# Performance work log

Hardware: AMD Instinct MI355X
Metric: run time of the kernel (lower is better)

## Reference

```python
import jax, jax.numpy as jnp
import numpy as np

K = 20
EPS = 1e-5
NEG_SLOPE = 0.2


def knn_idx(pts, k):
    # pts: [B, N, C] -> indices of k nearest neighbors [B, N, k]
    sq = jnp.sum(pts * pts, axis=-1)                     # [B, N]
    inner = jnp.einsum('bnc,bmc->bnm', pts, pts)         # [B, N, N]
    dist = sq[:, :, None] - 2.0 * inner + sq[:, None, :] # [B, N, N]
    _, idx = jax.lax.top_k(-dist, k)                     # nearest = smallest dist
    return idx


def batchnorm(h, gamma, beta):
    # h: [B, N, k, C]; normalize over (B, N, k) per channel (training-mode stats)
    mean = jnp.mean(h, axis=(0, 1, 2), keepdims=True)
    var = jnp.var(h, axis=(0, 1, 2), keepdims=True)
    return gamma * (h - mean) * jax.lax.rsqrt(var + EPS) + beta


def setup_inputs() -> dict:
    key = jax.random.key(0)
    ks = jax.random.split(key, 7)
    B, C, N = 8, 3, 4096
    x = jax.random.normal(ks[0], (B, C, N), dtype=jnp.float32)
    W1 = jax.random.normal(ks[1], (64, 6), dtype=jnp.float32) * (1.0 / np.sqrt(6.0))
    gamma1 = jnp.ones((64,), dtype=jnp.float32)
    beta1 = jnp.zeros((64,), dtype=jnp.float32)
    W2 = jax.random.normal(ks[2], (64, 64), dtype=jnp.float32) * (1.0 / 8.0)
    gamma2 = jnp.ones((64,), dtype=jnp.float32)
    beta2 = jnp.zeros((64,), dtype=jnp.float32)
    return {"x": x, "W1": W1, "gamma1": gamma1, "beta1": beta1,
            "W2": W2, "gamma2": gamma2, "beta2": beta2}


def reference(x, W1, gamma1, beta1, W2, gamma2, beta2):
    # x: [B, 3, N] point cloud
    pts = jnp.transpose(x, (0, 2, 1))                    # [B, N, 3]
    idx = knn_idx(pts, K)                                # [B, N, k]
    nbr = jax.vmap(lambda p, i: p[i])(pts, idx)          # [B, N, k, 3]
    center = pts[:, :, None, :]                          # [B, N, 1, 3]
    edge = jnp.concatenate(
        [nbr - center, jnp.broadcast_to(center, nbr.shape)], axis=-1)  # [B, N, k, 6]

    h = jnp.einsum('bnkc,oc->bnko', edge, W1)            # [B, N, k, 64]
    h = jax.nn.leaky_relu(batchnorm(h, gamma1, beta1), NEG_SLOPE)
    h = jnp.einsum('bnkc,oc->bnko', h, W2)               # [B, N, k, 64]
    h = jax.nn.leaky_relu(batchnorm(h, gamma2, beta2), NEG_SLOPE)

    out = jnp.max(h, axis=2)                             # max-pool over k neighbors
    return jnp.transpose(out, (0, 2, 1))                 # [B, 64, N]
```

## Files before the change

kernel.cpp:

```cpp
#include <hip/hip_runtime.h>
#include <hip/hip_bf16.h>
#include <math.h>

#define BB 8
#define NN 4096
#define KNN 20
#define CH 64
#define SAMPLES (BB*NN*KNN)
#define EPSF 1e-5f
#define SLOPE 0.2f
#define MCOPY 32

typedef float f32x4 __attribute__((ext_vector_type(4)));
typedef short bf16x8 __attribute__((ext_vector_type(8)));

__device__ __forceinline__ float key_decode(unsigned e) {
    return __uint_as_float((e & 0x80000000u) ? (e ^ 0x80000000u) : ~e);
}

__device__ __forceinline__ void rank_flush(unsigned long long* ovf,
                                           unsigned long long* inc,
                                           unsigned long long* scr,
                                           int& cnt, float& kthd, int lane) {
    while (cnt > 0) {
        int take = cnt < 44 ? cnt : 44;
        unsigned long long key;
        if (lane < take)      key = ovf[cnt - take + lane];
        else if (lane >= 44)  key = inc[lane - 44];
        else                  key = ~0ull;
        scr[lane] = key;
        __builtin_amdgcn_wave_barrier();
        int r = 0;
#pragma unroll
        for (int t = 0; t < 64; ++t) {
            unsigned long long kt = scr[t];
            r += (kt < key) ? 1 : 0;
        }
        __builtin_amdgcn_wave_barrier();
        if (r < KNN) inc[r] = key;
        __builtin_amdgcn_wave_barrier();
        kthd = key_decode((unsigned)(inc[KNN-1] >> 32));
        cnt -= take;
    }
}

__global__ __launch_bounds__(1024) void sort_kernel(const float* __restrict__ x,
        float4* __restrict__ pts4, float4* __restrict__ sp4, int* __restrict__ sidx,
        int* __restrict__ rankArr, double* __restrict__ zreg) {
#pragma clang fp contract(off)
    __shared__ unsigned long long S[NN];
    const int tid = threadIdx.x;
    const int b = blockIdx.x;
    if (b == 0 && tid < 992) zreg[tid] = 0.0;
    const float* xb = x + (size_t)b * 3 * NN;
    for (int i = tid; i < NN; i += 1024) {
        float mx = xb[i], my = xb[NN + i], mz = xb[2*NN + i];
        float sq = mx*mx; sq += my*my; sq += mz*mz;
        pts4[(b << 12) + i] = make_float4(-2.0f*mx, -2.0f*my, -2.0f*mz, sq);
        unsigned uu = __float_as_uint(mx);
        unsigned e = uu ^ (((unsigned)((int)uu >> 31)) | 0x80000000u);
        S[i] = ((unsigned long long)e << 32) | (unsigned)i;
    }
    __syncthreads();
    for (int k = 2; k <= NN; k <<= 1) {
        for (int j = k >> 1; j > 0; j >>= 1) {
#pragma unroll
            for (int tt = 0; tt < 2; ++tt) {
                int t = tid + tt*1024;
                int i = ((t & ~(j - 1)) << 1) | (t & (j - 1));
                int h = i | j;
                unsigned long long a = S[i], c = S[h];
                bool up = ((i & k) == 0);
                if ((a > c) == up) { S[i] = c; S[h] = a; }
            }
            __syncthreads();
        }
    }
    for (int s = tid; s < NN; s += 1024) {
        int oi = (int)(unsigned)(S[s] & 0xFFFFFFFFu);
        float mx = xb[oi], my = xb[NN + oi], mz = xb[2*NN + oi];
        float sq = mx*mx; sq += my*my; sq += mz*mz;
        sp4[(b << 12) + s] = make_float4(-2.0f*mx, -2.0f*my, -2.0f*mz, sq);
        sidx[(b << 12) + s] = oi;
        rankArr[(b << 12) + oi] = s;
    }
}

__global__ __launch_bounds__(256) void knn_kernel(const float4* __restrict__ pts4,
        const float4* __restrict__ sp4, const int* __restrict__ sidx,
        int* __restrict__ idx_out, double* __restrict__ mstats) {
#pragma clang fp contract(off)
    __shared__ unsigned long long OVF[4][160];
    __shared__ unsigned long long INC[4][24];
    __shared__ unsigned long long SCR[4][64];
    __shared__ float MOM[4][27];
    const int tid = threadIdx.x;
    const int lane = tid & 63;
    const int wv = __builtin_amdgcn_readfirstlane(tid >> 6);
    const int s = blockIdx.x * 4 + wv;
    const int b = s >> 12;
    const int ss = s & (NN - 1);
    const float4* sb = sp4 + ((size_t)b << 12);
    const int* si = sidx + ((size_t)b << 12);
    unsigned long long* ovf = &OVF[wv][0];
    unsigned long long* inc = &INC[wv][0];
    unsigned long long* scr = &SCR[wv][0];

    const float4 Qc = sb[ss];
    const float qx = -0.5f*Qc.x, qy = -0.5f*Qc.y, qz = -0.5f*Qc.z;
    const float sqn = Qc.w;
    int c0 = ss - 32; c0 = c0 < 0 ? 0 : (c0 > NN-64 ? NN-64 : c0);
    float kthd, thr, M;
    int cnt = 0;

    {
        const float4 P = sb[c0 + lane];
        const float mx = -0.5f*P.x, my = -0.5f*P.y, mz = -0.5f*P.z;
        float inner = qx*mx; inner += qy*my; inner += qz*mz;
        const float d = (sqn - 2.0f*inner) + P.w;
        unsigned uu = __float_as_uint(d);
        unsigned e = uu ^ (((unsigned)((int)uu >> 31)) | 0x80000000u);
        unsigned long long key = ((unsigned long long)e << 32) | (unsigned)si[c0 + lane];
        scr[lane] = key;
        __builtin_amdgcn_wave_barrier();
        int r = 0;
#pragma unroll
        for (int t = 0; t < 64; ++t) {
            unsigned long long kt = scr[t];
            r += (kt < key) ? 1 : 0;
        }
        __builtin_amdgcn_wave_barrier();
        if (r < KNN) inc[r] = key;
        __builtin_amdgcn_wave_barrier();
        kthd = key_decode((unsigned)(inc[KNN-1] >> 32));
        M = 1e-3f*(fabsf(kthd) + fabsf(sqn) + 1.0f);
        thr = (kthd - sqn) + M;
    }

    int lo = c0, hi = c0 + 64;
    bool dl = (lo == 0), dr = (hi == NN);

    float4 PL, PR;
    float xL = 0.f, xR = 0.f;
    if (!dl) {
        int st = lo - 64; st = st < 0 ? 0 : st;
        PL = sb[st + lane];
        xL = sb[lo - 1].x;
    }
    if (!dr) {
        int sI = hi + lane;
        PR = sb[sI < NN-1 ? sI : NN-1];
        xR = sb[hi].x;
    }

    while (!dl || !dr) {
        bool goL = false, goR = false;
        if (!dl) {
            const float dx = qx - (-0.5f*xL);
            goL = (dx*dx <= kthd + M);
            if (!goL) dl = true;
        }
        if (!dr) {
            const float dx = (-0.5f*xR) - qx;
            goR = (dx*dx <= kthd + M);
            if (!goR) dr = true;
        }
        const int stL = (lo - 64) < 0 ? 0 : (lo - 64);
        const int enR = (hi + 64) > NN ? NN : (hi + 64);

        float4 PLn = PL, PRn = PR;
        float xLn = 0.f, xRn = 0.f;
        if (goL && stL > 0) {
            int st2 = stL - 64; st2 = st2 < 0 ? 0 : st2;
            PLn = sb[st2 + lane];
            xLn = sb[stL - 1].x;
        }
        if (goR && enR < NN) {
            int sI = enR + lane;
            PRn = sb[sI < NN-1 ? sI : NN-1];
            xRn = sb[enR].x;
        }

        if (cnt > 32) {
            rank_flush(ovf, inc, scr, cnt, kthd, lane);
            M = 1e-3f*(fabsf(kthd) + fabsf(sqn) + 1.0f);
            thr = (kthd - sqn) + M;
        }

        if (goL) {
            const int sI = stL + lane;
            const bool valid = sI < lo;
            const float sc = fmaf(PL.x, qx, fmaf(PL.y, qy, fmaf(PL.z, qz, PL.w)));
            bool push = valid && (sc <= thr);
            unsigned long long mask = __ballot(push);
            if (mask) {
                if (push) {
                    const float mx = -0.5f*PL.x, my = -0.5f*PL.y, mz = -0.5f*PL.z;
                    float inner = qx*mx; inner += qy*my; inner += qz*mz;
                    const float d = (sqn - 2.0f*inner) + PL.w;
                    unsigned uu = __float_as_uint(d);
                    unsigned e = uu ^ (((unsigned)((int)uu >> 31)) | 0x80000000u);
                    unsigned long long key = ((unsigned long long)e << 32) | (unsigned)si[sI];
                    int ofs = (int)__popcll(mask & ((1ull << lane) - 1ull));
                    ovf[cnt + ofs] = key;
                }
                cnt += (int)__popcll(mask);
            }
            lo = stL;
            dl = (lo == 0);
            PL = PLn; xL = xLn;
        }
        if (goR) {
            const int sI = hi + lane;
            const int sa = sI < NN-1 ? sI : NN-1;
            const bool valid = sI < enR;
            const float sc = fmaf(PR.x, qx, fmaf(PR.y, qy, fmaf(PR.z, qz, PR.w)));
            bool push = valid && (sc <= thr);
            unsigned long long mask = __ballot(push);
            if (mask) {
                if (push) {
                    const float mx = -0.5f*PR.x, my = -0.5f*PR.y, mz = -0.5f*PR.z;
                    float inner = qx*mx; inner += qy*my; inner += qz*mz;
                    const float d = (sqn - 2.0f*inner) + PR.w;
                    unsigned uu = __float_as_uint(d);
                    unsigned e = uu ^ (((unsigned)((int)uu >> 31)) | 0x80000000u);
                    unsigned long long key = ((unsigned long long)e << 32) | (unsigned)si[sa];
                    int ofs = (int)__popcll(mask & ((1ull << lane) - 1ull));
                    ovf[cnt + ofs] = key;
                }
                cnt += (int)__popcll(mask);
            }
            hi = enR;
            dr = (hi == NN);
            PR = PRn; xR = xRn;
        }
    }
    rank_flush(ovf, inc, scr, cnt, kthd, lane);

    if (lane < KNN)
        idx_out[(size_t)s * KNN + lane] = (int)(unsigned)(inc[lane] & 0xFFFFFFFFull);

    float nx = 0.f, ny = 0.f, nz = 0.f, xx = 0.f, xy = 0.f, xz = 0.f,
          yy = 0.f, yz = 0.f, zz = 0.f;
    if (lane < KNN) {
        int nbr = (int)(unsigned)(inc[lane] & 0xFFFFFFFFull);
        float4 pn = pts4[(b << 12) + nbr];
        nx = -0.5f*pn.x; ny = -0.5f*pn.y; nz = -0.5f*pn.z;
        xx = nx*nx; xy = nx*ny; xz = nx*nz; yy = ny*ny; yz = ny*nz; zz = nz*nz;
    }
#pragma unroll
    for (int off = 32; off > 0; off >>= 1) {
        nx += __shfl_xor(nx, off); ny += __shfl_xor(ny, off); nz += __shfl_xor(nz, off);
        xx += __shfl_xor(xx, off); xy += __shfl_xor(xy, off); xz += __shfl_xor(xz, off);
        yy += __shfl_xor(yy, off); yz += __shfl_xor(yz, off); zz += __shfl_xor(zz, off);
    }
    if (lane == 0) {
        MOM[wv][0] = nx;  MOM[wv][1] = ny;  MOM[wv][2] = nz;
        MOM[wv][3] = qx;  MOM[wv][4] = qy;  MOM[wv][5] = qz;
        MOM[wv][6] = xx;  MOM[wv][7] = xy;  MOM[wv][8] = xz;
        MOM[wv][9] = yy;  MOM[wv][10] = yz; MOM[wv][11] = zz;
        MOM[wv][12] = nx*qx; MOM[wv][13] = nx*qy; MOM[wv][14] = nx*qz;
        MOM[wv][15] = ny*qx; MOM[wv][16] = ny*qy; MOM[wv][17] = ny*qz;
        MOM[wv][18] = nz*qx; MOM[wv][19] = nz*qy; MOM[wv][20] = nz*qz;
        MOM[wv][21] = qx*qx; MOM[wv][22] = qx*qy; MOM[wv][23] = qx*qz;
        MOM[wv][24] = qy*qy; MOM[wv][25] = qy*qz; MOM[wv][26] = qz*qz;
    }
    __syncthreads();
    if (tid < 27)
        atomicAdd(&mstats[(blockIdx.x & (MCOPY-1))*27 + tid],
                  (double)(MOM[0][tid] + MOM[1][tid] + MOM[2][tid] + MOM[3][tid]));
}

__device__ __forceinline__ void bsplit(float g, short& hi, short& lo) {
    unsigned bits = __float_as_uint(g);
    unsigned hbits = bits & 0xFFFF0000u;
    float rem = g - __uint_as_float(hbits);
    hi = (short)(bits >> 16);
    lo = (short)(__float_as_uint(rem) >> 16);
}

__global__ __launch_bounds__(256) void main_kernel(const int* __restrict__ idxb,
        const int* __restrict__ rankArr, const float4* __restrict__ pts4,
        const double* __restrict__ ms, const float* __restrict__ W1,
        const float* __restrict__ gamma1, const float* __restrict__ beta1,
        const float* __restrict__ W2,
        float* __restrict__ maxbuf, float* __restrict__ stats2f) {
    __shared__ __align__(16) short Thi[4][32*72];
    __shared__ __align__(16) short Tlo[4][32*72];
    __shared__ float chs[128];
    __shared__ float ab1s[128];
    __shared__ double msd[27];
    const int tid = threadIdx.x;
    const int lane = tid & 63;
    const int wv = __builtin_amdgcn_readfirstlane(tid >> 6);
    const int l15 = lane & 15;
    const int quad = lane >> 4;
    if (tid < 128) chs[tid] = 0.f;
    if (tid < 27) {
        double t = 0.0;
        for (int c = 0; c < MCOPY; ++c) t += ms[c*27 + tid];
        msd[tid] = t;
    }
    __syncthreads();
    if (tid < 64) {
        int c = tid;
        double wu[3], wvv[3];
#pragma unroll
        for (int i = 0; i < 3; ++i) {
            wu[i] = (double)W1[c*6 + i];
            wvv[i] = (double)W1[c*6 + 3 + i] - wu[i];
        }
        const double S = (double)SAMPLES;
        double mean = (wu[0]*msd[0] + wu[1]*msd[1] + wu[2]*msd[2]
                     + 20.0*(wvv[0]*msd[3] + wvv[1]*msd[4] + wvv[2]*msd[5])) / S;
        double qM1 = wu[0]*wu[0]*msd[6] + wu[1]*wu[1]*msd[9] + wu[2]*wu[2]*msd[11]
                   + 2.0*(wu[0]*wu[1]*msd[7] + wu[0]*wu[2]*msd[8] + wu[1]*wu[2]*msd[10]);
        double cross = 0.0;
#pragma unroll
        for (int i = 0; i < 3; ++i)
#pragma unroll
            for (int j = 0; j < 3; ++j)
                cross += wu[i] * msd[12 + i*3 + j] * wvv[j];
        double qpp = wvv[0]*wvv[0]*msd[21] + wvv[1]*wvv[1]*msd[24] + wvv[2]*wvv[2]*msd[26]
                   + 2.0*(wvv[0]*wvv[1]*msd[22] + wvv[0]*wvv[2]*msd[23] + wvv[1]*wvv[2]*msd[25]);
        double e2 = (qM1 + 2.0*cross + 20.0*qpp) / S;
        double var = e2 - mean*mean;
        float a = (float)((double)gamma1[c] / sqrt(var + (double)EPSF));
        ab1s[c] = a;
        ab1s[64 + c] = beta1[c] - a * (float)mean;
    }
    __syncthreads();

    bf16x8 whi[8], wlo[8];
#pragma unroll
    for (int t = 0; t < 4; ++t)
#pragma unroll
    for (int f = 0; f < 2; ++f) {
        const int o = 16*t + l15;
        const int c0 = 32*f + quad*8;
        const float4* wr = (const float4*)(W2 + o*64 + c0);
        float4 w0 = wr[0], w1 = wr[1];
        float vals[8] = {w0.x,w0.y,w0.z,w0.w,w1.x,w1.y,w1.z,w1.w};
        bf16x8 h, l;
#pragma unroll
        for (int j = 0; j < 8; ++j) { short hj, lj; bsplit(vals[j], hj, lj); h[j]=hj; l[j]=lj; }
        whi[t*2+f] = h; wlo[t*2+f] = l;
    }

    const float w10 = W1[lane*6+0], w11 = W1[lane*6+1], w12 = W1[lane*6+2];
    const float w13 = W1[lane*6+3], w14 = W1[lane*6+4], w15 = W1[lane*6+5];
    const float a1 = ab1s[lane], b1 = ab1s[64 + lane];
    float ssum[4] = {0.f,0.f,0.f,0.f}, ssq[4] = {0.f,0.f,0.f,0.f};
    float lm[4][4];
    short* thi = &Thi[wv][0];
    short* tlo = &Tlo[wv][0];

    const int pt0 = (blockIdx.x * 4 + wv) * 4;
    const int b = pt0 >> 12;
    const float4* pb = pts4 + ((size_t)b << 12);
    const int* rnk = rankArr + ((size_t)b << 12);

    for (int p = 0; p < 4; ++p) {
        const int pt = pt0 + p;
        const float4 pc = pb[pt & (NN - 1)];
        const float X = -0.5f*pc.x, Y = -0.5f*pc.y, Z = -0.5f*pc.z;
        const float vc = (w13 - w10)*X + (w14 - w11)*Y + (w15 - w12)*Z;
        const int srow = rnk[pt & (NN - 1)];
        const int* irow = idxb + ((size_t)((b << 12) + srow)) * KNN;
#pragma unroll
        for (int k = 0; k < KNN; ++k) {
            float4 pn = pb[irow[k]];
            float nx = -0.5f*pn.x, ny = -0.5f*pn.y, nz = -0.5f*pn.z;
            float uc = w10*nx + w11*ny + w12*nz;
            float g = a1 * (uc + vc) + b1;
            g = fmaxf(g, SLOPE * g);
            short hj, lj; bsplit(g, hj, lj);
            const int row = (k < 16) ? k : (16 + p*4 + (k - 16));
            thi[row*72 + lane] = hj;
            tlo[row*72 + lane] = lj;
        }
        __builtin_amdgcn_wave_barrier();

        bf16x8 ah1[2], al1[2];
#pragma unroll
        for (int f = 0; f < 2; ++f) {
            const int co = 32*f + quad*8;
            ah1[f] = *(const bf16x8*)&thi[l15*72 + co];
            al1[f] = *(const bf16x8*)&tlo[l15*72 + co];
        }

        f32x4 acc1[4];
#pragma unroll
        for (int t = 0; t < 4; ++t) acc1[t] = (f32x4)0.f;
#pragma unroll
        for (int t = 0; t < 4; ++t) {
#pragma unroll
            for (int f = 0; f < 2; ++f) {
                acc1[t] = __builtin_amdgcn_mfma_f32_16x16x32_bf16(ah1[f], whi[t*2+f], acc1[t], 0,0,0);
                acc1[t] = __builtin_amdgcn_mfma_f32_16x16x32_bf16(al1[f], whi[t*2+f], acc1[t], 0,0,0);
                acc1[t] = __builtin_amdgcn_mfma_f32_16x16x32_bf16(ah1[f], wlo[t*2+f], acc1[t], 0,0,0);
            }
        }
        __builtin_amdgcn_wave_barrier();

#pragma unroll
        for (int t = 0; t < 4; ++t) {
            float m1 = fmaxf(fmaxf(acc1[t][0], acc1[t][1]), fmaxf(acc1[t][2], acc1[t][3]));
            float s1 = acc1[t][0] + acc1[t][1] + acc1[t][2] + acc1[t][3];
            float q1 = acc1[t][0]*acc1[t][0] + acc1[t][1]*acc1[t][1]
                     + acc1[t][2]*acc1[t][2] + acc1[t][3]*acc1[t][3];
            m1 = fmaxf(m1, __shfl_xor(m1, 16)); m1 = fmaxf(m1, __shfl_xor(m1, 32));
            s1 += __shfl_xor(s1, 16); s1 += __shfl_xor(s1, 32);
            q1 += __shfl_xor(q1, 16); q1 += __shfl_xor(q1, 32);
            lm[p][t] = m1;
            ssum[t] += s1; ssq[t] += q1;
        }
    }

    {
        bf16x8 ah2[2], al2[2];
#pragma unroll
        for (int f = 0; f < 2; ++f) {
            const int co = 32*f + quad*8;
            ah2[f] = *(const bf16x8*)&thi[(16 + l15)*72 + co];
            al2[f] = *(const bf16x8*)&tlo[(16 + l15)*72 + co];
        }
        f32x4 accC[4];
#pragma unroll
        for (int t = 0; t < 4; ++t) accC[t] = (f32x4)0.f;
#pragma unroll
        for (int t = 0; t < 4; ++t) {
#pragma unroll
            for (int f = 0; f < 2; ++f) {
                accC[t] = __builtin_amdgcn_mfma_f32_16x16x32_bf16(ah2[f], whi[t*2+f], accC[t], 0,0,0);
                accC[t] = __builtin_amdgcn_mfma_f32_16x16x32_bf16(al2[f], whi[t*2+f], accC[t], 0,0,0);
                accC[t] = __builtin_amdgcn_mfma_f32_16x16x32_bf16(ah2[f], wlo[t*2+f], accC[t], 0,0,0);
            }
        }
#pragma unroll
        for (int t = 0; t < 4; ++t) {
            float cm = fmaxf(fmaxf(accC[t][0], accC[t][1]), fmaxf(accC[t][2], accC[t][3]));
            float cs = accC[t][0] + accC[t][1] + accC[t][2] + accC[t][3];
            float cq = accC[t][0]*accC[t][0] + accC[t][1]*accC[t][1]
                     + accC[t][2]*accC[t][2] + accC[t][3]*accC[t][3];
            float lmq = (quad == 0) ? lm[0][t] : (quad == 1) ? lm[1][t]
                      : (quad == 2) ? lm[2][t] : lm[3][t];
            maxbuf[((size_t)(pt0 + quad) << 6) + 16*t + l15] = fmaxf(lmq, cm);
            cs += __shfl_xor(cs, 16); cs += __shfl_xor(cs, 32);
            cq += __shfl_xor(cq, 16); cq += __shfl_xor(cq, 32);
            ssum[t] += cs; ssq[t] += cq;
        }
    }

    if (quad == 0) {
#pragma unroll
        for (int t = 0; t < 4; ++t) {
            atomicAdd(&chs[16*t + l15], ssum[t]);
            atomicAdd(&chs[64 + 16*t + l15], ssq[t]);
        }
    }
    __syncthreads();
    if (tid < 128)
        atomicAdd(&stats2f[(blockIdx.x & 1)*128 + tid], chs[tid]);
}

__global__ __launch_bounds__(256) void out_kernel(const float* __restrict__ maxbuf,
        const float* __restrict__ s2f, const float* __restrict__ gamma2,
        const float* __restrict__ beta2, float* __restrict__ out) {
    __shared__ float t[64][65];
    __shared__ float ab2s[128];
    const int tid = threadIdx.x;
    if (tid < 64) {
        int o = tid;
        double sum = (double)s2f[o] + (double)s2f[128 + o];
        double sq  = (double)s2f[64 + o] + (double)s2f[192 + o];
        double cnt = (double)SAMPLES;
        double mean = sum / cnt;
        double var  = sq / cnt - mean*mean;
        float a = (float)((double)gamma2[o] / sqrt(var + (double)EPSF));
        ab2s[o] = a;
        ab2s[64 + o] = beta2[o] - a * (float)mean;
    }
    const int b = blockIdx.x >> 6;
    const int n0 = (blockIdx.x & 63) << 6;
#pragma unroll
    for (int i = 0; i < 16; ++i) {
        int r = (tid >> 6) + i*4;
        int c = tid & 63;
        t[r][c] = maxbuf[(((size_t)((b << 12) + n0 + r)) << 6) + c];
    }
    __syncthreads();
#pragma unroll
    for (int i = 0; i < 16; ++i) {
        int o = (tid >> 6) + i*4;
        int nn = tid & 63;
        float a = ab2s[o], bb = ab2s[64 + o];
        float h = a * t[nn][o] + bb;
        out[(((size_t)(b*64 + o)) << 12) + n0 + nn] = h >= 0.f ? h : SLOPE*h;
    }
}

extern "C" void kernel_launch(void* const* d_in, const int* in_sizes, int n_in,
                              void* d_out, int out_size, void* d_ws, size_t ws_size,
                              hipStream_t stream) {
    const float* x      = (const float*)d_in[0];
    const float* W1     = (const float*)d_in[1];
    const float* gamma1 = (const float*)d_in[2];
    const float* beta1  = (const float*)d_in[3];
    const float* W2     = (const float*)d_in[4];
    const float* gamma2 = (const float*)d_in[5];
    const float* beta2  = (const float*)d_in[6];
    float* out = (float*)d_out;

    char* ws = (char*)d_ws;
    int*    idxb    = (int*)   (ws + 0);
    float4* pts4    = (float4*)(ws + 2621440);
    float4* sp4     = (float4*)(ws + 3145728);
    int*    sidx    = (int*)   (ws + 3670016);
    int*    rankArr = (int*)   (ws + 3801088);
    float*  maxbuf  = (float*) (ws + 19398656);
    double* mstats  = (double*)(ws + 27787264);
    float*  stats2f = (float*) (ws + 27794176);
    double* zreg    = (double*)(ws + 27787264);

    sort_kernel <<<8, 1024, 0, stream>>>(x, pts4, sp4, sidx, rankArr, zreg);
    knn_kernel  <<<8192, 256, 0, stream>>>(pts4, sp4, sidx, idxb, mstats);
    main_kernel <<<2048, 256, 0, stream>>>(idxb, rankArr, pts4, mstats, W1, gamma1,
                                           beta1, W2, maxbuf, stats2f);
    out_kernel  <<<512, 256, 0, stream>>>(maxbuf, stats2f, gamma2, beta2, out);
}
```

Baseline: 256.8 us.

## Map one kNN query per lane with shared candidate chunks and per-lane insertion sort

The kNN kernel changes from one wave per query, with lanes as candidates and a 64-way rank sort for merging, to one wave handling 64 consecutive sorted queries, one per lane. Candidate chunks of 64 points are staged in LDS and scanned by every lane. Survivors go into a per-lane buffer that is merged into a per-lane top-20 list by insertion sort. The aim is to drop the cross-lane rank passes and the per-query scheduling overhead. The cost is wider union windows across queries, divergent insertion sorts, a large LDS footprint and only 512 single-wave blocks, which leaves the GPU lightly occupied.

Result: slower. 665.3 us (+159.0%).

```diff
diff --git a/kernel.cpp b/kernel.cpp
--- a/kernel.cpp
+++ b/kernel.cpp
@@ -16,32 +16,6 @@
 
 __device__ __forceinline__ float key_decode(unsigned e) {
     return __uint_as_float((e & 0x80000000u) ? (e ^ 0x80000000u) : ~e);
-}
-
-__device__ __forceinline__ void rank_flush(unsigned long long* ovf,
-                                           unsigned long long* inc,
-                                           unsigned long long* scr,
-                                           int& cnt, float& kthd, int lane) {
-    while (cnt > 0) {
-        int take = cnt < 44 ? cnt : 44;
-        unsigned long long key;
-        if (lane < take)      key = ovf[cnt - take + lane];
-        else if (lane >= 44)  key = inc[lane - 44];
-        else                  key = ~0ull;
-        scr[lane] = key;
-        __builtin_amdgcn_wave_barrier();
-        int r = 0;
-#pragma unroll
-        for (int t = 0; t < 64; ++t) {
-            unsigned long long kt = scr[t];
-            r += (kt < key) ? 1 : 0;
-        }
-        __builtin_amdgcn_wave_barrier();
-        if (r < KNN) inc[r] = key;
-        __builtin_amdgcn_wave_barrier();
-        kthd = key_decode((unsigned)(inc[KNN-1] >> 32));
-        cnt -= take;
-    }
 }
 
 __global__ __launch_bounds__(1024) void sort_kernel(const float* __restrict__ x,
@@ -86,189 +60,190 @@
     }
 }
 
-__global__ __launch_bounds__(256) void knn_kernel(const float4* __restrict__ pts4,
+
+#define BCAP 80
+
+__device__ __forceinline__ void lane_flush(unsigned long long* BUF,
+        unsigned long long* INC, const int lane, int& cnt, int& m,
+        float& kthd, const float sqn, float& M, float& thr) {
+    for (int j = 0; j < cnt; ++j) {
+        unsigned long long key = BUF[(j << 6) + lane];
+        if (m < KNN) {
+            int i = m - 1;
+            while (i >= 0 && INC[(i << 6) + lane] > key) {
+                INC[((i + 1) << 6) + lane] = INC[(i << 6) + lane]; --i;
+            }
+            INC[((i + 1) << 6) + lane] = key; ++m;
+        } else if (key < INC[((KNN - 1) << 6) + lane]) {
+            int i = KNN - 2;
+            while (i >= 0 && INC[(i << 6) + lane] > key) {
+                INC[((i + 1) << 6) + lane] = INC[(i << 6) + lane]; --i;
+            }
+            INC[((i + 1) << 6) + lane] = key;
+        }
+    }
+    cnt = 0;
+    if (m == KNN) {
+        kthd = key_decode((unsigned)(INC[((KNN - 1) << 6) + lane] >> 32));
+        M = 1e-3f*(fabsf(kthd) + fabsf(sqn) + 1.0f);
+        thr = (kthd - sqn) + M;
+    }
+}
+
+__device__ __forceinline__ void eval_chunk(const float4* ch, const int* sic,
+        unsigned long long* BUF, const int lane, const float qx, const float qy,
+        const float qz, const float sqn, const float thr, int& cnt) {
+#pragma clang fp contract(off)
+#pragma unroll 8
+    for (int t = 0; t < 64; ++t) {
+        const float4 P = ch[t];
+        const float sc = fmaf(P.x, qx, fmaf(P.y, qy, fmaf(P.z, qz, P.w)));
+        const bool push = sc <= thr;
+        if (__any(push)) {
+            const float mx = -0.5f*P.x, my = -0.5f*P.y, mz = -0.5f*P.z;
+            float inner = qx*mx; inner += qy*my; inner += qz*mz;
+            const float d = (sqn - 2.0f*inner) + P.w;
+            unsigned uu = __float_as_uint(d);
+            unsigned e = uu ^ (((unsigned)((int)uu >> 31)) | 0x80000000u);
+            unsigned long long key = ((unsigned long long)e << 32) | (unsigned)sic[t];
+            if (push) { BUF[(cnt << 6) + lane] = key; ++cnt; }
+        }
+    }
+}
+
+__global__ __launch_bounds__(64) void knn_kernel(const float4* __restrict__ pts4,
         const float4* __restrict__ sp4, const int* __restrict__ sidx,
         int* __restrict__ idx_out, double* __restrict__ mstats) {
 #pragma clang fp contract(off)
-    __shared__ unsigned long long OVF[4][160];
-    __shared__ unsigned long long INC[4][24];
-    __shared__ unsigned long long SCR[4][64];
-    __shared__ float MOM[4][27];
-    const int tid = threadIdx.x;
-    const int lane = tid & 63;
-    const int wv = __builtin_amdgcn_readfirstlane(tid >> 6);
-    const int s = blockIdx.x * 4 + wv;
-    const int b = s >> 12;
-    const int ss = s & (NN - 1);
+    __shared__ float4 CHK[2][64];
+    __shared__ int    SIc[2][64];
+    __shared__ unsigned long long BUF[BCAP*64];
+    __shared__ unsigned long long INC[KNN*64];
+
+    const int lane = threadIdx.x;
+    const int Q0 = blockIdx.x << 6;
+    const int b  = Q0 >> 12;
+    const int r0 = Q0 & (NN - 1);
     const float4* sb = sp4 + ((size_t)b << 12);
-    const int* si = sidx + ((size_t)b << 12);
-    unsigned long long* ovf = &OVF[wv][0];
-    unsigned long long* inc = &INC[wv][0];
-    unsigned long long* scr = &SCR[wv][0];
-
-    const float4 Qc = sb[ss];
-    const float qx = -0.5f*Qc.x, qy = -0.5f*Qc.y, qz = -0.5f*Qc.z;
-    const float sqn = Qc.w;
-    int c0 = ss - 32; c0 = c0 < 0 ? 0 : (c0 > NN-64 ? NN-64 : c0);
-    float kthd, thr, M;
-    int cnt = 0;
-
-    {
-        const float4 P = sb[c0 + lane];
-        const float mx = -0.5f*P.x, my = -0.5f*P.y, mz = -0.5f*P.z;
-        float inner = qx*mx; inner += qy*my; inner += qz*mz;
-        const float d = (sqn - 2.0f*inner) + P.w;
-        unsigned uu = __float_as_uint(d);
-        unsigned e = uu ^ (((unsigned)((int)uu >> 31)) | 0x80000000u);
-        unsigned long long key = ((unsigned long long)e << 32) | (unsigned)si[c0 + lane];
-        scr[lane] = key;
-        __builtin_amdgcn_wave_barrier();
-        int r = 0;
-#pragma unroll
-        for (int t = 0; t < 64; ++t) {
-            unsigned long long kt = scr[t];
-            r += (kt < key) ? 1 : 0;
-        }
-        __builtin_amdgcn_wave_barrier();
-        if (r < KNN) inc[r] = key;
-        __builtin_amdgcn_wave_barrier();
-        kthd = key_decode((unsigned)(inc[KNN-1] >> 32));
-        M = 1e-3f*(fabsf(kthd) + fabsf(sqn) + 1.0f);
-        thr = (kthd - sqn) + M;
-    }
-
-    int lo = c0, hi = c0 + 64;
+    const int*    si = sidx + ((size_t)b << 12);
+
+    const float4 R0 = sb[r0 + lane];
+    const int    Ri0 = si[r0 + lane];
+    const float qx = -0.5f*R0.x, qy = -0.5f*R0.y, qz = -0.5f*R0.z;
+    const float sqn = R0.w;
+
+    int lo = r0, hi = r0 + 64;
     bool dl = (lo == 0), dr = (hi == NN);
 
-    float4 PL, PR;
-    float xL = 0.f, xR = 0.f;
+    CHK[0][lane] = R0; SIc[0][lane] = Ri0;
+    __builtin_amdgcn_wave_barrier();
+
+    float4 RL, RR; int RiL = 0, RiR = 0;
+    int stL = 0, enR = NN;
     if (!dl) {
-        int st = lo - 64; st = st < 0 ? 0 : st;
-        PL = sb[st + lane];
-        xL = sb[lo - 1].x;
+        stL = lo - 64; if (stL < 0) stL = 0;
+        int ii = stL + lane; int ia = ii < lo ? ii : lo - 1;
+        RL = sb[ia]; RiL = si[ia];
     }
     if (!dr) {
-        int sI = hi + lane;
-        PR = sb[sI < NN-1 ? sI : NN-1];
-        xR = sb[hi].x;
-    }
+        enR = hi + 64; if (enR > NN) enR = NN;
+        int ii = hi + lane; int ia = ii < NN - 1 ? ii : NN - 1;
+        RR = sb[ia]; RiR = si[ia];
+    }
+
+    float kthd = INFINITY, M = INFINITY, thr = INFINITY;
+    int cnt = 0, m = 0;
+
+    eval_chunk(&CHK[0][0], &SIc[0][0], BUF, lane, qx, qy, qz, sqn, thr, cnt);
 
     while (!dl || !dr) {
-        bool goL = false, goR = false;
         if (!dl) {
-            const float dx = qx - (-0.5f*xL);
-            goL = (dx*dx <= kthd + M);
-            if (!goL) dl = true;
+            const float xl = -0.5f * __shfl(RL.x, lo - 1 - stL);
+            const float dx = qx - xl;
+            if (__all(dx*dx > kthd + M)) dl = true;
+            else {
+                const bool v = (stL + lane) < lo;
+                __builtin_amdgcn_wave_barrier();
+                CHK[0][lane] = v ? RL : make_float4(0.f, 0.f, 0.f, INFINITY);
+                SIc[0][lane] = v ? RiL : 0;
+                __builtin_amdgcn_wave_barrier();
+                const int lo2 = stL;
+                const bool dl2 = (lo2 == 0);
+                int stL2 = lo2 - 64; if (stL2 < 0) stL2 = 0;
+                if (!dl2) {
+                    int ii = stL2 + lane; int ia = ii < lo2 ? ii : lo2 - 1;
+                    RL = sb[ia]; RiL = si[ia];
+                }
+                if (__any(cnt > 16))
+                    lane_flush(BUF, INC, lane, cnt, m, kthd, sqn, M, thr);
+                eval_chunk(&CHK[0][0], &SIc[0][0], BUF, lane, qx, qy, qz, sqn, thr, cnt);
+                lo = lo2; stL = stL2; dl = dl2;
+            }
         }
         if (!dr) {
-            const float dx = (-0.5f*xR) - qx;
-            goR = (dx*dx <= kthd + M);
-            if (!goR) dr = true;
-        }
-        const int stL = (lo - 64) < 0 ? 0 : (lo - 64);
-        const int enR = (hi + 64) > NN ? NN : (hi + 64);
-
-        float4 PLn = PL, PRn = PR;
-        float xLn = 0.f, xRn = 0.f;
-        if (goL && stL > 0) {
-            int st2 = stL - 64; st2 = st2 < 0 ? 0 : st2;
-            PLn = sb[st2 + lane];
-            xLn = sb[stL - 1].x;
-        }
-        if (goR && enR < NN) {
-            int sI = enR + lane;
-            PRn = sb[sI < NN-1 ? sI : NN-1];
-            xRn = sb[enR].x;
-        }
-
-        if (cnt > 32) {
-            rank_flush(ovf, inc, scr, cnt, kthd, lane);
-            M = 1e-3f*(fabsf(kthd) + fabsf(sqn) + 1.0f);
-            thr = (kthd - sqn) + M;
-        }
-
-        if (goL) {
-            const int sI = stL + lane;
-            const bool valid = sI < lo;
-            const float sc = fmaf(PL.x, qx, fmaf(PL.y, qy, fmaf(PL.z, qz, PL.w)));
-            bool push = valid && (sc <= thr);
-            unsigned long long mask = __ballot(push);
-            if (mask) {
-                if (push) {
-                    const float mx = -0.5f*PL.x, my = -0.5f*PL.y, mz = -0.5f*PL.z;
-                    float inner = qx*mx; inner += qy*my; inner += qz*mz;
-                    const float d = (sqn - 2.0f*inner) + PL.w;
-                    unsigned uu = __float_as_uint(d);
-                    unsigned e = uu ^ (((unsigned)((int)uu >> 31)) | 0x80000000u);
-                    unsigned long long key = ((unsigned long long)e << 32) | (unsigned)si[sI];
-                    int ofs = (int)__popcll(mask & ((1ull << lane) - 1ull));
-                    ovf[cnt + ofs] = key;
+            const float xr = -0.5f * __shfl(RR.x, 0);
+            const float dx = xr - qx;
+            if (__all(dx*dx > kthd + M)) dr = true;
+            else {
+                const bool v = (hi + lane) < enR;
+                __builtin_amdgcn_wave_barrier();
+                CHK[1][lane] = v ? RR : make_float4(0.f, 0.f, 0.f, INFINITY);
+                SIc[1][lane] = v ? RiR : 0;
+                __builtin_amdgcn_wave_barrier();
+                const int hi2 = enR;
+                const bool dr2 = (hi2 == NN);
+                int enR2 = hi2 + 64; if (enR2 > NN) enR2 = NN;
+                if (!dr2) {
+                    int ii = hi2 + lane; int ia = ii < NN - 1 ? ii : NN - 1;
+                    RR = sb[ia]; RiR = si[ia];
                 }
-                cnt += (int)__popcll(mask);
-            }
-            lo = stL;
-            dl = (lo == 0);
-            PL = PLn; xL = xLn;
-        }
-        if (goR) {
-            const int sI = hi + lane;
-            const int sa = sI < NN-1 ? sI : NN-1;
-            const bool valid = sI < enR;
-            const float sc = fmaf(PR.x, qx, fmaf(PR.y, qy, fmaf(PR.z, qz, PR.w)));
-            bool push = valid && (sc <= thr);
-            unsigned long long mask = __ballot(push);
-            if (mask) {
-                if (push) {
-                    const float mx = -0.5f*PR.x, my = -0.5f*PR.y, mz = -0.5f*PR.z;
-                    float inner = qx*mx; inner += qy*my; inner += qz*mz;
-                    const float d = (sqn - 2.0f*inner) + PR.w;
-                    unsigned uu = __float_as_uint(d);
-                    unsigned e = uu ^ (((unsigned)((int)uu >> 31)) | 0x80000000u);
-                    unsigned long long key = ((unsigned long long)e << 32) | (unsigned)si[sa];
-                    int ofs = (int)__popcll(mask & ((1ull << lane) - 1ull));
-                    ovf[cnt + ofs] = key;
-                }
-                cnt += (int)__popcll(mask);
-            }
-            hi = enR;
-            dr = (hi == NN);
-            PR = PRn; xR = xRn;
-        }
-    }
-    rank_flush(ovf, inc, scr, cnt, kthd, lane);
-
-    if (lane < KNN)
-        idx_out[(size_t)s * KNN + lane] = (int)(unsigned)(inc[lane] & 0xFFFFFFFFull);
-
-    float nx = 0.f, ny = 0.f, nz = 0.f, xx = 0.f, xy = 0.f, xz = 0.f,
-          yy = 0.f, yz = 0.f, zz = 0.f;
-    if (lane < KNN) {
-        int nbr = (int)(unsigned)(inc[lane] & 0xFFFFFFFFull);
-        float4 pn = pts4[(b << 12) + nbr];
-        nx = -0.5f*pn.x; ny = -0.5f*pn.y; nz = -0.5f*pn.z;
-        xx = nx*nx; xy = nx*ny; xz = nx*nz; yy = ny*ny; yz = ny*nz; zz = nz*nz;
-    }
-#pragma unroll
-    for (int off = 32; off > 0; off >>= 1) {
-        nx += __shfl_xor(nx, off); ny += __shfl_xor(ny, off); nz += __shfl_xor(nz, off);
-        xx += __shfl_xor(xx, off); xy += __shfl_xor(xy, off); xz += __shfl_xor(xz, off);
-        yy += __shfl_xor(yy, off); yz += __shfl_xor(yz, off); zz += __shfl_xor(zz, off);
-    }
-    if (lane == 0) {
-        MOM[wv][0] = nx;  MOM[wv][1] = ny;  MOM[wv][2] = nz;
-        MOM[wv][3] = qx;  MOM[wv][4] = qy;  MOM[wv][5] = qz;
-        MOM[wv][6] = xx;  MOM[wv][7] = xy;  MOM[wv][8] = xz;
-        MOM[wv][9] = yy;  MOM[wv][10] = yz; MOM[wv][11] = zz;
-        MOM[wv][12] = nx*qx; MOM[wv][13] = nx*qy; MOM[wv][14] = nx*qz;
-        MOM[wv][15] = ny*qx; MOM[wv][16] = ny*qy; MOM[wv][17] = ny*qz;
-        MOM[wv][18] = nz*qx; MOM[wv][19] = nz*qy; MOM[wv][20] = nz*qz;
-        MOM[wv][21] = qx*qx; MOM[wv][22] = qx*qy; MOM[wv][23] = qx*qz;
-        MOM[wv][24] = qy*qy; MOM[wv][25] = qy*qz; MOM[wv][26] = qz*qz;
-    }
-    __syncthreads();
-    if (tid < 27)
-        atomicAdd(&mstats[(blockIdx.x & (MCOPY-1))*27 + tid],
-                  (double)(MOM[0][tid] + MOM[1][tid] + MOM[2][tid] + MOM[3][tid]));
+                if (__any(cnt > 16))
+                    lane_flush(BUF, INC, lane, cnt, m, kthd, sqn, M, thr);
+                eval_chunk(&CHK[1][0], &SIc[1][0], BUF, lane, qx, qy, qz, sqn, thr, cnt);
+                hi = hi2; enR = enR2; dr = dr2;
+            }
+        }
+    }
+    lane_flush(BUF, INC, lane, cnt, m, kthd, sqn, M, thr);
+
+    unsigned* TB = (unsigned*)BUF;
+#pragma unroll
+    for (int j = 0; j < KNN; ++j)
+        TB[lane*21 + j] = (unsigned)(INC[(j << 6) + lane] & 0xFFFFFFFFull);
+    __builtin_amdgcn_wave_barrier();
+    int* iout = idx_out + (size_t)Q0 * KNN;
+#pragma unroll
+    for (int u = 0; u < KNN; ++u) {
+        int g = (u << 6) + lane;
+        iout[g] = (int)TB[(g / KNN)*21 + (g % KNN)];
+    }
+
+    const float4* pb = pts4 + ((size_t)b << 12);
+    float nx=0.f, ny=0.f, nz=0.f, xx=0.f, xy=0.f, xz=0.f, yy=0.f, yz=0.f, zz=0.f;
+#pragma unroll
+    for (int j = 0; j < KNN; ++j) {
+        int nb = (int)(INC[(j << 6) + lane] & 0xFFFFFFFFull);
+        float4 pn = pb[nb];
+        float ax = -0.5f*pn.x, ay = -0.5f*pn.y, az = -0.5f*pn.z;
+        nx += ax; ny += ay; nz += az;
+        xx += ax*ax; xy += ax*ay; xz += ax*az;
+        yy += ay*ay; yz += ay*az; zz += az*az;
+    }
+    double* msd = &mstats[(blockIdx.x & (MCOPY-1))*27];
+#define RED27(v, i) { float r_ = (v); \
+    r_ += __shfl_xor(r_, 1);  r_ += __shfl_xor(r_, 2);  r_ += __shfl_xor(r_, 4); \
+    r_ += __shfl_xor(r_, 8);  r_ += __shfl_xor(r_, 16); r_ += __shfl_xor(r_, 32); \
+    if (lane == 0) atomicAdd(&msd[i], (double)r_); }
+    RED27(nx, 0) RED27(ny, 1) RED27(nz, 2)
+    RED27(qx, 3) RED27(qy, 4) RED27(qz, 5)
+    RED27(xx, 6) RED27(xy, 7) RED27(xz, 8)
+    RED27(yy, 9) RED27(yz, 10) RED27(zz, 11)
+    RED27(nx*qx, 12) RED27(nx*qy, 13) RED27(nx*qz, 14)
+    RED27(ny*qx, 15) RED27(ny*qy, 16) RED27(ny*qz, 17)
+    RED27(nz*qx, 18) RED27(nz*qy, 19) RED27(nz*qz, 20)
+    RED27(qx*qx, 21) RED27(qx*qy, 22) RED27(qx*qz, 23)
+    RED27(qy*qy, 24) RED27(qy*qz, 25) RED27(qz*qz, 26)
+#undef RED27
 }
 
 __device__ __forceinline__ void bsplit(float g, short& hi, short& lo) {
@@ -524,7 +499,7 @@
     double* zreg    = (double*)(ws + 27787264);
 
     sort_kernel <<<8, 1024, 0, stream>>>(x, pts4, sp4, sidx, rankArr, zreg);
-    knn_kernel  <<<8192, 256, 0, stream>>>(pts4, sp4, sidx, idxb, mstats);
+    knn_kernel  <<<512, 64, 0, stream>>>(pts4, sp4, sidx, idxb, mstats);
     main_kernel <<<2048, 256, 0, stream>>>(idxb, rankArr, pts4, mstats, W1, gamma1,
                                            beta1, W2, maxbuf, stats2f);
     out_kernel  <<<512, 256, 0, stream>>>(maxbuf, stats2f, gamma2, beta2, out);
```
